# Optimization experiments

Measured on AMD Instinct MI355X. Metric: run time of the kernel, lower is better.

Reference implementation:

```python
import jax, jax.numpy as jnp
import numpy as np

NUM_HEADS = 16

def setup_inputs() -> dict:
    key = jax.random.key(0)
    ks = jax.random.split(key, 5)
    B, T, C = 2, 2048, 1024
    s = 0.02
    return {
        "x": jax.random.normal(ks[0], (B, T, C), dtype=jnp.float32),
        "attn_w": jax.random.normal(ks[1], (3 * C, C), dtype=jnp.float32) * s,
        "attn_b": jax.random.normal(ks[2], (3 * C,), dtype=jnp.float32) * s,
        "proj_w": jax.random.normal(ks[3], (C, C), dtype=jnp.float32) * s,
        "proj_b": jax.random.normal(ks[4], (C,), dtype=jnp.float32) * s,
    }

def reference(x, attn_w, attn_b, proj_w, proj_b):
    B, T, C = x.shape
    H = NUM_HEADS
    D = C // H
    # fused QKV projection (torch Linear: x @ W^T + b)
    qkv = x @ attn_w.T + attn_b                      # [B, T, 3C]
    q, k, v = jnp.split(qkv, 3, axis=-1)             # each [B, T, C]
    # split heads -> [B, H, T, D]
    def heads(t):
        return t.reshape(B, T, H, D).transpose(0, 2, 1, 3)
    q, k, v = heads(q), heads(k), heads(v)
    scale = 1.0 / jnp.sqrt(jnp.asarray(D, dtype=x.dtype))
    scores = jnp.einsum("bhtd,bhsd->bhts", q, k) * scale   # [B, H, T, T]
    causal = jnp.tril(jnp.ones((T, T), dtype=bool))
    scores = jnp.where(causal[None, None], scores, jnp.asarray(-jnp.inf, dtype=scores.dtype))
    att = jax.nn.softmax(scores, axis=-1)
    out = jnp.einsum("bhts,bhsd->bhtd", att, v)      # [B, H, T, D]
    out = out.transpose(0, 2, 1, 3).reshape(B, T, C)
    return out @ proj_w.T + proj_b
```

## Files before the change

kernel.cpp:

```cpp
#include <hip/hip_runtime.h>
#include <hip/hip_bf16.h>

typedef __bf16 bf16_t;
typedef __bf16 bf16x4 __attribute__((ext_vector_type(4)));
typedef __bf16 bf16x8 __attribute__((ext_vector_type(8)));
typedef float f32x4 __attribute__((ext_vector_type(4)));
typedef float f32x8 __attribute__((ext_vector_type(8)));

#define MFMA16(a, b, c) __builtin_amdgcn_mfma_f32_16x16x32_bf16(a, b, c, 0, 0, 0)

#define GLOAD_LDS16(g, l)                                              \
  __builtin_amdgcn_global_load_lds(                                    \
      (const __attribute__((address_space(1))) unsigned int*)(g),      \
      (__attribute__((address_space(3))) unsigned int*)(l), 16, 0, 0)

constexpr int B = 2, T = 2048, C = 1024, H = 16, D = 64;
constexpr int NQKV = 3 * C;
constexpr int M = B * T;

#define QSCALE 0.18033688011112042f

__global__ __launch_bounds__(256) void cvt_kernel(
    const float* __restrict__ s0, bf16_t* __restrict__ d0, int n0,
    const float* __restrict__ s1, bf16_t* __restrict__ d1, int n1,
    const float* __restrict__ s2, bf16_t* __restrict__ d2, int n2)
{
  const float* s; bf16_t* d; int n;
  if (blockIdx.y == 0)      { s = s0; d = d0; n = n0; }
  else if (blockIdx.y == 1) { s = s1; d = d1; n = n1; }
  else                      { s = s2; d = d2; n = n2; }
  const int idx = (blockIdx.x * 256 + threadIdx.x) * 8;
  if (idx >= n) return;
  f32x8 t = *(const f32x8*)(s + idx);
  bf16x8 r;
#pragma unroll
  for (int j = 0; j < 8; ++j) r[j] = (bf16_t)t[j];
  *(bf16x8*)(d + idx) = r;
}

template<int BM, int BN, int MI, int NI>
__device__ __forceinline__ void gemm_mainloop_db(
    const bf16_t* __restrict__ A, const bf16_t* __restrict__ Wt,
    const int K, const int m0, const int n0,
    bf16_t* ldsA0, bf16_t* ldsA1, bf16_t* ldsB0, bf16_t* ldsB1,
    f32x4 acc[MI][NI])
{
  const int tid  = threadIdx.x;
  const int wv   = tid >> 6;
  const int lane = tid & 63;
  const int col  = lane & 15;
  const int quad = lane >> 4;
  const int lr8  = lane >> 3;
  const int cpos = lane & 7;
  const int wm = wv >> 1, wn = wv & 1;
  constexpr int AJ = BM / 32;
  constexpr int ARW = BM / 4;
  constexpr int BJ = BN / 32;
  constexpr int BRW = BN / 4;

  const bf16_t* ag[AJ]; const bf16_t* bg[BJ];
#pragma unroll
  for (int j = 0; j < AJ; ++j)
    ag[j] = A + (size_t)(m0 + wv * ARW + j * 8 + lr8) * K + (cpos ^ lr8) * 8;
#pragma unroll
  for (int j = 0; j < BJ; ++j)
    bg[j] = Wt + (size_t)(n0 + wv * BRW + j * 8 + lr8) * K + (cpos ^ lr8) * 8;

  const int xa = quad ^ (col & 7);
  const int niter = K / 64;

#pragma unroll
  for (int j = 0; j < AJ; ++j)
    GLOAD_LDS16(ag[j], ldsA0 + (wv * ARW + j * 8) * 64);
#pragma unroll
  for (int j = 0; j < BJ; ++j)
    GLOAD_LDS16(bg[j], ldsB0 + (wv * BRW + j * 8) * 64);

  for (int it = 0; it < niter; ++it) {
    __syncthreads();
    const bf16_t* cA = (it & 1) ? ldsA1 : ldsA0;
    const bf16_t* cB = (it & 1) ? ldsB1 : ldsB0;
    if (it + 1 < niter) {
      bf16_t* nA = (it & 1) ? ldsA0 : ldsA1;
      bf16_t* nB = (it & 1) ? ldsB0 : ldsB1;
      const int off = (it + 1) * 64;
#pragma unroll
      for (int j = 0; j < AJ; ++j)
        GLOAD_LDS16(ag[j] + off, nA + (wv * ARW + j * 8) * 64);
#pragma unroll
      for (int j = 0; j < BJ; ++j)
        GLOAD_LDS16(bg[j] + off, nB + (wv * BRW + j * 8) * 64);
    }
#pragma unroll
    for (int ks = 0; ks < 2; ++ks) {
      const int xk = (xa ^ (ks * 4)) * 8;
      bf16x8 af[MI], bfr[NI];
#pragma unroll
      for (int mi = 0; mi < MI; ++mi)
        af[mi] = *(const bf16x8*)(cA + (wm * (MI * 16) + mi * 16 + col) * 64 + xk);
#pragma unroll
      for (int ni = 0; ni < NI; ++ni)
        bfr[ni] = *(const bf16x8*)(cB + (wn * (NI * 16) + ni * 16 + col) * 64 + xk);
#pragma unroll
      for (int mi = 0; mi < MI; ++mi)
#pragma unroll
        for (int ni = 0; ni < NI; ++ni)
          acc[mi][ni] = MFMA16(af[mi], bfr[ni], acc[mi][ni]);
    }
  }
}

__global__ __launch_bounds__(256) void qkv_gemm_kernel(
    const bf16_t* __restrict__ x, const bf16_t* __restrict__ w,
    const float* __restrict__ bias,
    bf16_t* __restrict__ qws, bf16_t* __restrict__ kws, bf16_t* __restrict__ vws)
{
  __shared__ __align__(16) bf16_t ldsA[2][128 * 64];
  __shared__ __align__(16) bf16_t ldsB[2][128 * 64];
  const int lane = threadIdx.x & 63;
  const int wv   = threadIdx.x >> 6;
  const int col  = lane & 15;
  const int quad = lane >> 4;
  const int wm = wv >> 1, wn = wv & 1;
  const int m0 = blockIdx.y * 128;
  const int n0 = blockIdx.x * 128;

  f32x4 acc[4][4] = {};
  gemm_mainloop_db<128, 128, 4, 4>(x, w, C, m0, n0,
                                   ldsA[0], ldsA[1], ldsB[0], ldsB[1], acc);

  const int which = n0 >> 10;

  if (which == 2) {
    __syncthreads();
    bf16_t* vt = &ldsA[0][0] + wv * 4096;

#pragma unroll
    for (int ni = 0; ni < 4; ++ni) {
      const int n = n0 + wn * 64 + ni * 16 + col;
      const float bval = bias[n];
      const int dl = ni * 16 + col;
#pragma unroll
      for (int r = 0; r < 4; ++r) {
        bf16x4 pw;
#pragma unroll
        for (int mi = 0; mi < 4; ++mi)
          pw[mi] = (bf16_t)(acc[mi][ni][r] + bval);
        const int k = 2 * quad + (r >> 1);
        const int S = dl * 8 + (k ^ (dl & 7));
        *(bf16x4*)(vt + S * 8 + (r & 1) * 4) = pw;
      }
    }

    const int b   = (m0 + wm * 64) >> 11;
    const int t0w = (m0 + wm * 64) & (T - 1);
    const int h   = ((n0 + wn * 64) & (C - 1)) >> 6;
    const size_t bh = (size_t)(b * H + h);
    const int lr8 = lane >> 3;
    const int c8  = lane & 7;
#pragma unroll
    for (int j = 0; j < 8; ++j) {
      const int dl = j * 8 + lr8;
      const int d  = dl;
      bf16x8 row = *(const bf16x8*)(vt + (dl * 8 + (c8 ^ (dl & 7))) * 8);
      *(bf16x8*)(vws + (bh * D + d) * T + t0w + c8 * 8) = row;
    }
  } else {
#pragma unroll
    for (int ni = 0; ni < 4; ++ni) {
      const int n = n0 + wn * 64 + ni * 16 + col;
      const float bval = bias[n];
      const int c = n & (C - 1);
      const int h = c >> 6;
      const int d = c & 63;
#pragma unroll
      for (int mi = 0; mi < 4; ++mi) {
#pragma unroll
        for (int r = 0; r < 4; ++r) {
          const int m = m0 + wm * 64 + mi * 16 + quad * 4 + r;
          const int b = m >> 11;
          const int t = m & (T - 1);
          const size_t bh = (size_t)(b * H + h);
          if (which == 0)
            qws[(bh * T + t) * D + d] = (bf16_t)((acc[mi][ni][r] + bval) * QSCALE);
          else
            kws[(bh * T + t) * D + d] = (bf16_t)(acc[mi][ni][r] + bval);
        }
      }
    }
  }
}

__global__ __launch_bounds__(256) void attn_kernel(
    const bf16_t* __restrict__ qws, const bf16_t* __restrict__ kws,
    const bf16_t* __restrict__ vws, bf16_t* __restrict__ yws)
{
  const int id = blockIdx.x;
  const int bh = id & 31;
  const int qt = 31 - (id >> 5);
  const int tid  = threadIdx.x;
  const int wv   = tid >> 6;
  const int lane = tid & 63;
  const int col  = lane & 15;
  const int quad = lane >> 4;

  const bf16_t* Q  = qws + (size_t)bh * T * D;
  const bf16_t* K  = kws + (size_t)bh * T * D;
  const bf16_t* Vt = vws + (size_t)bh * D * T;

  __shared__ __align__(16) bf16_t ldsK[2][64 * 64];
  __shared__ __align__(16) bf16_t ldsV[2][64 * 64];
  __shared__ __align__(16) bf16_t ldsP_s[4][16 * 64];
  bf16_t* ldsPw = ldsP_s[wv];

  const int xs   = col & 7;
  const int cxq  = (quad ^ xs) * 8;
  const int lr8  = lane >> 3;
  const int ksrc = (lane & 7) ^ lr8;
  const int pxor = (quad & 1) * 4;
  const int b = bh >> 4;
  const int h = bh & 15;

  const int t0 = qt * 64;
  const int tw = t0 + 16 * wv;

  bf16x8 qf0 = *(const bf16x8*)(Q + (size_t)(tw + col) * D + quad * 8);
  bf16x8 qf1 = *(const bf16x8*)(Q + (size_t)(tw + col) * D + 32 + quad * 8);

  f32x4 o[4] = {};
  f32x4 lp = {};

  auto stage = [&](int it) {
    const int sn = it * 64;
    bf16_t* dK = ldsK[it & 1];
    bf16_t* dV = ldsV[it & 1];
#pragma unroll
    for (int j = 0; j < 2; ++j) {
      GLOAD_LDS16(K + (size_t)(sn + 16 * wv + j * 8 + lr8) * D + ksrc * 8,
                  dK + (16 * wv + j * 8) * 64);
      GLOAD_LDS16(Vt + (size_t)(16 * wv + j * 8 + lr8) * T + sn + ksrc * 8,
                  dV + (16 * wv + j * 8) * 64);
    }
  };

  auto compute_tile = [&](const bf16_t* bK, const bf16_t* bV, int s0,
                          bool diag) {
    f32x4 sc[4];
    __builtin_amdgcn_s_setprio(1);
#pragma unroll
    for (int kb = 0; kb < 4; ++kb) {
      const bf16_t* kr = bK + (kb * 16 + col) * 64;
      bf16x8 kf0 = *(const bf16x8*)(kr + cxq);
      bf16x8 kf1 = *(const bf16x8*)(kr + (cxq ^ 32));
      f32x4 a = {};
      a = MFMA16(qf0, kf0, a);
      a = MFMA16(qf1, kf1, a);
      sc[kb] = a;
    }
    __builtin_amdgcn_s_setprio(0);
#pragma unroll
    for (int r = 0; r < 4; ++r) {
      const int prow = (quad * 4 + r) * 64;
      const int pxr  = pxor + r;
      bf16x4 pw;
#pragma unroll
      for (int kb = 0; kb < 4; ++kb) {
        float p = __builtin_amdgcn_exp2f(sc[kb][r]);
        if (diag && (s0 + kb * 16 + col > tw + quad * 4 + r)) p = 0.0f;
        lp[r] += p;
        pw[kb] = (bf16_t)p;
      }
      *(bf16x4*)(ldsPw + prow + (((col >> 1) ^ pxr) * 8) + (col & 1) * 4) = pw;
    }
    __builtin_amdgcn_s_setprio(1);
#pragma unroll
    for (int ks = 0; ks < 2; ++ks) {
      const int xk = cxq ^ (ks * 32);
      bf16x8 pa = *(const bf16x8*)(ldsPw + col * 64 + xk);
#pragma unroll
      for (int ni = 0; ni < 4; ++ni) {
        bf16x8 vf = *(const bf16x8*)(bV + (ni * 16 + col) * 64 + xk);
        o[ni] = MFMA16(pa, vf, o[ni]);
      }
    }
    __builtin_amdgcn_s_setprio(0);
  };

  stage(0);

  for (int it = 0; it < qt; ++it) {
    __syncthreads();
    stage(it + 1);
    compute_tile(ldsK[it & 1], ldsV[it & 1], it * 64, false);
  }
  {
    __syncthreads();
    compute_tile(ldsK[qt & 1], ldsV[qt & 1], qt * 64, true);
  }

#pragma unroll
  for (int r = 0; r < 4; ++r) {
    float l0 = lp[r];
#pragma unroll
    for (int off = 1; off < 16; off <<= 1)
      l0 += __shfl_xor(l0, off);
    const float rl0 = 1.0f / l0;
    const int th = tw + quad * 4 + r;
#pragma unroll
    for (int ni = 0; ni < 4; ++ni) {
      const int d = ni * 16 + col;
      yws[((size_t)(b * T + th)) * C + h * D + d] = (bf16_t)(o[ni][r] * rl0);
    }
  }
}

__global__ __launch_bounds__(256) void proj_gemm_kernel(
    const bf16_t* __restrict__ y, const bf16_t* __restrict__ w,
    const float* __restrict__ bias, float* __restrict__ out)
{
  __shared__ __align__(16) bf16_t ldsA[2][128 * 64];
  __shared__ __align__(16) bf16_t ldsB[2][64 * 64];
  const int lane = threadIdx.x & 63;
  const int wv   = threadIdx.x >> 6;
  const int col  = lane & 15;
  const int quad = lane >> 4;
  const int wm = wv >> 1, wn = wv & 1;
  const int m0 = blockIdx.y * 128;
  const int n0 = blockIdx.x * 64;

  f32x4 acc[4][2] = {};
  gemm_mainloop_db<128, 64, 4, 2>(y, w, C, m0, n0,
                                  ldsA[0], ldsA[1], ldsB[0], ldsB[1], acc);

#pragma unroll
  for (int ni = 0; ni < 2; ++ni) {
    const int n = n0 + wn * 32 + ni * 16 + col;
    const float bval = bias[n];
#pragma unroll
    for (int mi = 0; mi < 4; ++mi) {
#pragma unroll
      for (int r = 0; r < 4; ++r) {
        const int m = m0 + wm * 64 + mi * 16 + quad * 4 + r;
        out[(size_t)m * C + n] = acc[mi][ni][r] + bval;
      }
    }
  }
}

extern "C" void kernel_launch(void* const* d_in, const int* in_sizes, int n_in,
                              void* d_out, int out_size, void* d_ws, size_t ws_size,
                              hipStream_t stream) {
  const float* x      = (const float*)d_in[0];
  const float* attn_w = (const float*)d_in[1];
  const float* attn_b = (const float*)d_in[2];
  const float* proj_w = (const float*)d_in[3];
  const float* proj_b = (const float*)d_in[4];
  float* out = (float*)d_out;

  const size_t E = (size_t)B * H * T * D;
  char* ws = (char*)d_ws;
  bf16_t* qws = (bf16_t*)(ws);
  bf16_t* kws = (bf16_t*)(ws + 2 * E);
  bf16_t* vws = (bf16_t*)(ws + 4 * E);
  bf16_t* yws = (bf16_t*)(ws + 6 * E);
  bf16_t* xb  = (bf16_t*)(ws + 8 * E);
  bf16_t* awb = (bf16_t*)(ws + 10 * E);
  bf16_t* pwb = (bf16_t*)(ws + 11 * E + E / 2);

  const int NX = M * C, NAW = NQKV * C, NPW = C * C;
  cvt_kernel<<<dim3(NX / 2048, 3), 256, 0, stream>>>(
      x, xb, NX, attn_w, awb, NAW, proj_w, pwb, NPW);
  qkv_gemm_kernel<<<dim3(NQKV / 128, M / 128), 256, 0, stream>>>(
      xb, awb, attn_b, qws, kws, vws);
  attn_kernel<<<1024, 256, 0, stream>>>(qws, kws, vws, yws);
  proj_gemm_kernel<<<dim3(C / 64, M / 128), 256, 0, stream>>>(
      yws, pwb, proj_b, out);
}
```

Baseline: 169.0 us.

## Process four causal query tiles per attention block to share K/V loads

Each attention workgroup now handles four query tiles (gi, 15-gi, 16+gi, 31-gi) that together give every block the same amount of causal work, and loads each K/V tile once for all query tiles still active. This cuts K/V global-to-LDS traffic and launches a quarter as many blocks. In exchange it holds far more accumulators in registers, which may lower occupancy or cause spills, and with only 256 blocks the GPU may be underfilled.

```diff
diff --git a/kernel.cpp b/kernel.cpp
--- a/kernel.cpp
+++ b/kernel.cpp
@@ -19,6 +19,8 @@
 constexpr int M = B * T;
 
 #define QSCALE 0.18033688011112042f
+
+template<int N> struct IC { static constexpr int value = N; };
 
 __global__ __launch_bounds__(256) void cvt_kernel(
     const float* __restrict__ s0, bf16_t* __restrict__ d0, int n0,
@@ -197,7 +199,7 @@
 {
   const int id = blockIdx.x;
   const int bh = id & 31;
-  const int qt = 31 - (id >> 5);
+  const int gi = id >> 5;
   const int tid  = threadIdx.x;
   const int wv   = tid >> 6;
   const int lane = tid & 63;
@@ -210,8 +212,7 @@
 
   __shared__ __align__(16) bf16_t ldsK[2][64 * 64];
   __shared__ __align__(16) bf16_t ldsV[2][64 * 64];
-  __shared__ __align__(16) bf16_t ldsP_s[4][16 * 64];
-  bf16_t* ldsPw = ldsP_s[wv];
+  __shared__ __align__(16) bf16_t ldsP_s[4][4][16 * 64];
 
   const int xs   = col & 7;
   const int cxq  = (quad ^ xs) * 8;
@@ -221,14 +222,22 @@
   const int b = bh >> 4;
   const int h = bh & 15;
 
-  const int t0 = qt * 64;
-  const int tw = t0 + 16 * wv;
-
-  bf16x8 qf0 = *(const bf16x8*)(Q + (size_t)(tw + col) * D + quad * 8);
-  bf16x8 qf1 = *(const bf16x8*)(Q + (size_t)(tw + col) * D + 32 + quad * 8);
-
-  f32x4 o[4] = {};
-  f32x4 lp = {};
+  const int qa = gi, qb = 15 - gi, qc = 16 + gi, qd = 31 - gi;
+  const int qt[4] = { qd, qc, qb, qa };
+
+  int tw[4];
+  bf16x8 qf[4][2];
+  bf16_t* Pp[4];
+#pragma unroll
+  for (int t = 0; t < 4; ++t) {
+    tw[t] = qt[t] * 64 + 16 * wv;
+    qf[t][0] = *(const bf16x8*)(Q + (size_t)(tw[t] + col) * D + quad * 8);
+    qf[t][1] = *(const bf16x8*)(Q + (size_t)(tw[t] + col) * D + 32 + quad * 8);
+    Pp[t] = ldsP_s[t][wv];
+  }
+
+  f32x4 o[4][4] = {};
+  f32x4 lp[4] = {};
 
   auto stage = [&](int it) {
     const int sn = it * 64;
@@ -243,44 +252,58 @@
     }
   };
 
-  auto compute_tile = [&](const bf16_t* bK, const bf16_t* bV, int s0,
-                          bool diag) {
-    f32x4 sc[4];
+  auto body = [&](auto NTC, const bf16_t* bK, const bf16_t* bV,
+                  int s0, bool diag) {
+    constexpr int NT = decltype(NTC)::value;
+    f32x4 sc[NT][4];
     __builtin_amdgcn_s_setprio(1);
 #pragma unroll
     for (int kb = 0; kb < 4; ++kb) {
       const bf16_t* kr = bK + (kb * 16 + col) * 64;
       bf16x8 kf0 = *(const bf16x8*)(kr + cxq);
       bf16x8 kf1 = *(const bf16x8*)(kr + (cxq ^ 32));
-      f32x4 a = {};
-      a = MFMA16(qf0, kf0, a);
-      a = MFMA16(qf1, kf1, a);
-      sc[kb] = a;
+#pragma unroll
+      for (int t = 0; t < NT; ++t) {
+        f32x4 a = {};
+        a = MFMA16(qf[t][0], kf0, a);
+        a = MFMA16(qf[t][1], kf1, a);
+        sc[t][kb] = a;
+      }
     }
     __builtin_amdgcn_s_setprio(0);
 #pragma unroll
-    for (int r = 0; r < 4; ++r) {
-      const int prow = (quad * 4 + r) * 64;
-      const int pxr  = pxor + r;
-      bf16x4 pw;
-#pragma unroll
-      for (int kb = 0; kb < 4; ++kb) {
-        float p = __builtin_amdgcn_exp2f(sc[kb][r]);
-        if (diag && (s0 + kb * 16 + col > tw + quad * 4 + r)) p = 0.0f;
-        lp[r] += p;
-        pw[kb] = (bf16_t)p;
-      }
-      *(bf16x4*)(ldsPw + prow + (((col >> 1) ^ pxr) * 8) + (col & 1) * 4) = pw;
+    for (int t = 0; t < NT; ++t) {
+      const bool dg = diag && (t == NT - 1);
+#pragma unroll
+      for (int r = 0; r < 4; ++r) {
+        const int prow = (quad * 4 + r) * 64;
+        const int pxr  = pxor + r;
+        const int poff = prow + (((col >> 1) ^ pxr) * 8) + (col & 1) * 4;
+        bf16x4 pw;
+#pragma unroll
+        for (int kb = 0; kb < 4; ++kb) {
+          float p = __builtin_amdgcn_exp2f(sc[t][kb][r]);
+          if (dg && (s0 + kb * 16 + col > tw[t] + quad * 4 + r)) p = 0.0f;
+          lp[t][r] += p;
+          pw[kb] = (bf16_t)p;
+        }
+        *(bf16x4*)(Pp[t] + poff) = pw;
+      }
     }
     __builtin_amdgcn_s_setprio(1);
 #pragma unroll
     for (int ks = 0; ks < 2; ++ks) {
       const int xk = cxq ^ (ks * 32);
-      bf16x8 pa = *(const bf16x8*)(ldsPw + col * 64 + xk);
+      bf16x8 pa[NT];
+#pragma unroll
+      for (int t = 0; t < NT; ++t)
+        pa[t] = *(const bf16x8*)(Pp[t] + col * 64 + xk);
 #pragma unroll
       for (int ni = 0; ni < 4; ++ni) {
         bf16x8 vf = *(const bf16x8*)(bV + (ni * 16 + col) * 64 + xk);
-        o[ni] = MFMA16(pa, vf, o[ni]);
+#pragma unroll
+        for (int t = 0; t < NT; ++t)
+          o[t][ni] = MFMA16(pa[t], vf, o[t][ni]);
       }
     }
     __builtin_amdgcn_s_setprio(0);
@@ -288,28 +311,43 @@
 
   stage(0);
 
-  for (int it = 0; it < qt; ++it) {
-    __syncthreads();
-    stage(it + 1);
-    compute_tile(ldsK[it & 1], ldsV[it & 1], it * 64, false);
-  }
-  {
-    __syncthreads();
-    compute_tile(ldsK[qt & 1], ldsV[qt & 1], qt * 64, true);
-  }
-
-#pragma unroll
-  for (int r = 0; r < 4; ++r) {
-    float l0 = lp[r];
-#pragma unroll
-    for (int off = 1; off < 16; off <<= 1)
-      l0 += __shfl_xor(l0, off);
-    const float rl0 = 1.0f / l0;
-    const int th = tw + quad * 4 + r;
-#pragma unroll
-    for (int ni = 0; ni < 4; ++ni) {
-      const int d = ni * 16 + col;
-      yws[((size_t)(b * T + th)) * C + h * D + d] = (bf16_t)(o[ni][r] * rl0);
+  int it = 0;
+  for (; it <= qa; ++it) {
+    __syncthreads();
+    if (it + 1 <= qd) stage(it + 1);
+    body(IC<4>{}, ldsK[it & 1], ldsV[it & 1], it * 64, it == qa);
+  }
+  for (; it <= qb; ++it) {
+    __syncthreads();
+    if (it + 1 <= qd) stage(it + 1);
+    body(IC<3>{}, ldsK[it & 1], ldsV[it & 1], it * 64, it == qb);
+  }
+  for (; it <= qc; ++it) {
+    __syncthreads();
+    if (it + 1 <= qd) stage(it + 1);
+    body(IC<2>{}, ldsK[it & 1], ldsV[it & 1], it * 64, it == qc);
+  }
+  for (; it <= qd; ++it) {
+    __syncthreads();
+    if (it + 1 <= qd) stage(it + 1);
+    body(IC<1>{}, ldsK[it & 1], ldsV[it & 1], it * 64, it == qd);
+  }
+
+#pragma unroll
+  for (int t = 0; t < 4; ++t) {
+#pragma unroll
+    for (int r = 0; r < 4; ++r) {
+      float l0 = lp[t][r];
+#pragma unroll
+      for (int off = 1; off < 16; off <<= 1)
+        l0 += __shfl_xor(l0, off);
+      const float rl0 = 1.0f / l0;
+      const int th = tw[t] + quad * 4 + r;
+#pragma unroll
+      for (int ni = 0; ni < 4; ++ni) {
+        const int d = ni * 16 + col;
+        yws[((size_t)(b * T + th)) * C + h * D + d] = (bf16_t)(o[t][ni][r] * rl0);
+      }
     }
   }
 }
@@ -372,7 +410,7 @@
       x, xb, NX, attn_w, awb, NAW, proj_w, pwb, NPW);
   qkv_gemm_kernel<<<dim3(NQKV / 128, M / 128), 256, 0, stream>>>(
       xb, awb, attn_b, qws, kws, vws);
-  attn_kernel<<<1024, 256, 0, stream>>>(qws, kws, vws, yws);
+  attn_kernel<<<256, 256, 0, stream>>>(qws, kws, vws, yws);
   proj_gemm_kernel<<<dim3(C / 64, M / 128), 256, 0, stream>>>(
       yws, pwb, proj_b, out);
 }
```

New measurement: 175.7 us. 4.0% more time.
